# Performance work log

Hardware: AMD Instinct MI355X
Metric: run time of the kernel (lower is better)

The kernel has to match this reference:

```python
import jax, jax.numpy as jnp
import numpy as np

B, S, N, M = 64, 512, 512, 128   # batch, sensory_size, state_size, motor_size
UNFOLDS = 6
DT = 0.1  # elapsed_time


def _gate(v, mu, sigma):
    # piecewise-linear 'sigmoid': clip((v - mu + sigma) / (2 sigma), 0, 1)
    # v: [B, P] -> [B, P, 1] broadcast against [P, N]
    return jnp.clip((v[..., None] - mu + sigma) / (2.0 * sigma), 0.0, 1.0)


def setup_inputs() -> dict:
    key = jax.random.key(0)
    ks = jax.random.split(key, 12)
    u = lambda k, sh, lo, hi: jax.random.uniform(k, sh, jnp.float32, lo, hi)
    inputs = jax.random.normal(ks[0], (B, S), dtype=jnp.float32)
    states = jax.random.normal(ks[1], (B, N), dtype=jnp.float32) * 0.1
    # parameters per _init_ranges
    tau = u(ks[2], (N,), 0.001, 2.0)
    b = u(ks[3], (N,), -0.2, 0.2)
    erev = jnp.where(jax.random.bernoulli(ks[4], 0.8, (N, N)), 1.0, -1.0).astype(jnp.float32)
    w = u(ks[5], (N, N), 0.001, 1.0)
    sigma = jnp.full((N, N), 0.5, jnp.float32)
    mu = jnp.full((N, N), 0.5, jnp.float32)
    sensory_erev = jnp.where(jax.random.bernoulli(ks[6], 0.8, (S, N)), 1.0, -1.0).astype(jnp.float32)
    sensory_w = u(ks[7], (S, N), 0.001, 1.0)
    sensory_sigma = jnp.full((S, N), 0.5, jnp.float32)
    sensory_mu = jnp.full((S, N), 0.5, jnp.float32)
    sparsity_mask = jax.random.bernoulli(ks[8], 0.3, (N, N)).astype(jnp.float32)
    sensory_sparsity_mask = jax.random.bernoulli(ks[9], 0.3, (S, N)).astype(jnp.float32)
    input_w = jnp.ones((S,), jnp.float32)
    input_b = jnp.zeros((S,), jnp.float32)
    output_w = jnp.ones((M,), jnp.float32)
    output_b = jnp.zeros((M,), jnp.float32)
    return dict(inputs=inputs, states=states, tau=tau, b=b, erev=erev, w=w,
                sigma=sigma, mu=mu, sensory_erev=sensory_erev, sensory_w=sensory_w,
                sensory_sigma=sensory_sigma, sensory_mu=sensory_mu,
                sparsity_mask=sparsity_mask, sensory_sparsity_mask=sensory_sparsity_mask,
                input_w=input_w, input_b=input_b, output_w=output_w, output_b=output_b)


def reference(inputs, states, tau, b, erev, w, sigma, mu,
              sensory_erev, sensory_w, sensory_sigma, sensory_mu,
              sparsity_mask, sensory_sparsity_mask,
              input_w, input_b, output_w, output_b):
    # input mapping (affine)
    x = inputs * input_w + input_b                                   # [B, S]
    # sensory synapses, computed once
    sa = _gate(x, sensory_mu, sensory_sigma) * sensory_sparsity_mask  # [B, S, N]
    s_rev = jnp.einsum('bsn,sn->bn', sa, sensory_erev)               # [B, N]
    s_w = jnp.einsum('bsn,sn->bn', sa, sensory_w)                    # [B, N]
    delta = DT / UNFOLDS

    def step(v, _):
        g = _gate(v, mu, sigma) * sparsity_mask                      # [B, N, N]
        sum_rev = jnp.einsum('bij,ij->bj', g, erev) + s_rev + b      # sum over presynaptic i
        sum_w = jnp.einsum('bij,ij->bj', g, w) + s_w
        k = 1.0 / (1.0 + sum_w)
        taun = tau * k
        q = taun / (taun + delta)
        v_new = q * v + (1.0 - q) * k * sum_rev
        return v_new, None

    v, _ = jax.lax.scan(step, states, None, length=UNFOLDS)
    # output mapping: slice last M neurons (M < N), then affine
    out = v[:, -M:] * output_w + output_b                            # [B, M]
    return out, v
```

## Files before the change

kernel.cpp:

```cpp
#include <hip/hip_runtime.h>

constexpr int cB = 64, cS = 512, cN = 512, cM = 128, cUNF = 6;
constexpr float cDELTA = 0.016666666666666666f;

constexpr int KB = 4;
constexpr int JT = 32;
constexpr int NJT = cN / JT;
constexpr int NT = 1024;
constexpr int NW = NT / 64;
constexpr int NB = (cB / KB) * NJT;

constexpr int ILEN = 8;
constexpr int SLEN = 16;

constexpr int SM_EW    = 0;
constexpr int SM_STAGE = cN * JT * 2;
constexpr int SM_REDR  = SM_STAGE + cN * KB;
constexpr int SM_REDW  = SM_REDR + KB * NW * JT;
constexpr int SM_FLOATS = SM_REDW + KB * NW * JT;
constexpr size_t SMEM_BYTES = (size_t)SM_FLOATS * 4;

constexpr size_t OFF_EWT = 0;
constexpr size_t OFF_SRB = (size_t)cN * cN * 2;
constexpr size_t OFF_SW  = OFF_SRB + (size_t)cB * cN;
constexpr size_t OFF_VA  = OFF_SW  + (size_t)cB * cN;
constexpr size_t OFF_VB  = OFF_VA  + (size_t)cB * cN;
constexpr size_t OFF_CTR = OFF_VB  + (size_t)cB * cN;
constexpr int CTR_INTS = 256 + 16;

__device__ __forceinline__ float clamp01(float x) {
    return __builtin_amdgcn_fmed3f(x, 0.0f, 1.0f);
}

__global__ __launch_bounds__(NT)
void k_prep(const float* __restrict__ inputs, const float* __restrict__ bias,
            const float* __restrict__ erev,  const float* __restrict__ wgt,
            const float* __restrict__ sigma, const float* __restrict__ mu,
            const float* __restrict__ serev, const float* __restrict__ swgt,
            const float* __restrict__ ssigma,const float* __restrict__ smu,
            const float* __restrict__ mask,  const float* __restrict__ smask,
            const float* __restrict__ inw,   const float* __restrict__ inb,
            float* __restrict__ ws)
{
    float2* EWt  = (float2*)(ws + OFF_EWT);
    float*  srb  = ws + OFF_SRB;
    float*  swS  = ws + OFF_SW;
    int*    ctr  = (int*)(ws + OFF_CTR);
    int*    flags = ctr + 256;

    const int tid = threadIdx.x, bid = blockIdx.x;
    const int bg = bid >> 4, jt = bid & (NJT - 1);
    const int b0 = bg * KB, j0 = jt * JT;
    const int jl = tid & (JT - 1), ic = tid >> 5;
    const int wv_id = tid >> 6, lane = tid & 63;
    const int j = j0 + jl;

    __shared__ float xsh[cS * KB];
    __shared__ float redR[KB * NW * JT];
    __shared__ float redW[KB * NW * JT];

    {
        int idx = bid * NT + tid;
        int i = idx >> 9, jj = idx & (cN - 1);
        int jtt = jj >> 5, jjl = jj & (JT - 1);
        float mk = mask[idx];
        EWt[(size_t)jtt * (cN * JT) + i * JT + jjl] =
            make_float2(erev[idx] * mk, wgt[idx] * mk);
        if (mk != 0.0f && !((sigma[idx] == 0.5f) && (mu[idx] == 0.5f)))
            atomicOr(&flags[jtt], 1);
    }

#pragma unroll
    for (int r = 0; r < (cS * KB) / NT; ++r) {
        int t = tid + r * NT;
        int bb = t & 3, s = t >> 2;
        xsh[t] = fmaf(inputs[(b0 + bb) * cS + s], inw[s], inb[s]);
    }
    __syncthreads();

    {
        float aR[KB] = {0.f, 0.f, 0.f, 0.f}, aW[KB] = {0.f, 0.f, 0.f, 0.f};
        int idx = (ic * SLEN) * cN + j;
        int xo  = (ic * SLEN) * KB;
#pragma unroll 4
        for (int ii = 0; ii < SLEN; ++ii, idx += cN, xo += KB) {
            float sg = ssigma[idx];
            float a  = 0.5f / sg;
            float c  = fmaf(-smu[idx], a, 0.5f);
            float mk = smask[idx];
            float e  = serev[idx] * mk;
            float wv = swgt[idx] * mk;
            const float4 xv = *(const float4*)&xsh[xo];
            float g;
            g = clamp01(fmaf(xv.x, a, c)); aR[0] = fmaf(g, e, aR[0]); aW[0] = fmaf(g, wv, aW[0]);
            g = clamp01(fmaf(xv.y, a, c)); aR[1] = fmaf(g, e, aR[1]); aW[1] = fmaf(g, wv, aW[1]);
            g = clamp01(fmaf(xv.z, a, c)); aR[2] = fmaf(g, e, aR[2]); aW[2] = fmaf(g, wv, aW[2]);
            g = clamp01(fmaf(xv.w, a, c)); aR[3] = fmaf(g, e, aR[3]); aW[3] = fmaf(g, wv, aW[3]);
        }
#pragma unroll
        for (int b = 0; b < KB; ++b) {
            aR[b] += __shfl_xor(aR[b], 32, 64);
            aW[b] += __shfl_xor(aW[b], 32, 64);
        }
        if (lane < JT) {
#pragma unroll
            for (int b = 0; b < KB; ++b) {
                redR[(b * NW + wv_id) * JT + jl] = aR[b];
                redW[(b * NW + wv_id) * JT + jl] = aW[b];
            }
        }
    }
    __syncthreads();

    if (tid < JT * KB) {
        int jj = tid & (JT - 1), bb = tid >> 5;
        float r = 0.f, wv = 0.f;
#pragma unroll
        for (int w = 0; w < NW; ++w) {
            r  += redR[(bb * NW + w) * JT + jj];
            wv += redW[(bb * NW + w) * JT + jj];
        }
        int jg = j0 + jj;
        int gidx = (b0 + bb) * cN + jg;
        srb[gidx] = r + bias[jg];
        swS[gidx] = wv;
    }
}

__global__ __launch_bounds__(NT)
void k_main(const float* __restrict__ states, const float* __restrict__ tau,
            const float* __restrict__ sigma,  const float* __restrict__ mu,
            const float* __restrict__ outw,   const float* __restrict__ outb,
            float* __restrict__ out, float* __restrict__ ws)
{
    extern __shared__ float smem[];
    float*  ewlf  = smem + SM_EW;
    float*  stage = smem + SM_STAGE;
    float*  redR  = smem + SM_REDR;
    float*  redW  = smem + SM_REDW;

    const float* srb = ws + OFF_SRB;
    const float* swS = ws + OFF_SW;
    float* vA  = ws + OFF_VA;
    float* vB  = ws + OFF_VB;
    int*   ctr = (int*)(ws + OFF_CTR);

    const int tid = threadIdx.x, bid = blockIdx.x;
    const int jt = (bid & 7) * 2 + ((bid >> 3) & 1);
    const int bg = bid >> 4;
    const int b0 = bg * KB, j0 = jt * JT;
    const int jp = tid & 15;
    const int ic = tid >> 4;
    const int wv_id = tid >> 6, lane = tid & 63;
    int* barU  = ctr + bg * 16;
    const int* flags = ctr + 256;

    {
        const float4* gsrc = (const float4*)(ws + OFF_EWT) + (size_t)jt * (cN * JT / 2);
        float4* ldst = (float4*)ewlf;
#pragma unroll 2
        for (int k = 0; k < 8; ++k)
            ldst[k * NT + tid] = gsrc[k * NT + tid];
    }
    const int fast = (flags[jt] == 0);

    float my_srb = 0.f, my_sw = 0.f, my_tau = 0.f, my_ow = 0.f, my_ob = 0.f;
    int my_gidx = 0, my_mi = -1;
    if (tid < JT * KB) {
        int jj = tid & (JT - 1), bb = tid >> 5;
        int jg = j0 + jj;
        my_gidx = (b0 + bb) * cN + jg;
        my_srb  = srb[my_gidx];
        my_sw   = swS[my_gidx];
        my_tau  = tau[jg];
        if (jg >= cN - cM) {
            int m = jg - (cN - cM);
            my_ow = outw[m]; my_ob = outb[m];
            my_mi = (b0 + bb) * cM + m;
        }
    }

    const float* vin = states;
    for (int u = 0; u < cUNF; ++u) {
        float* vout = (u == cUNF - 1) ? (out + cB * cM) : ((u & 1) ? vA : vB);

#pragma unroll
        for (int r = 0; r < (cN * KB) / NT; ++r) {
            int t = tid + r * NT;
            int bb = t & 3, ii = t >> 2;
            float vvv = __hip_atomic_load(&vin[(b0 + bb) * cN + ii],
                                          __ATOMIC_RELAXED, __HIP_MEMORY_SCOPE_AGENT);
            stage[t] = fast ? clamp01(vvv) : vvv;
        }
        __syncthreads();

        float vold = 0.f;
        if (tid < JT * KB)
            vold = __hip_atomic_load(&vin[my_gidx],
                                     __ATOMIC_RELAXED, __HIP_MEMORY_SCOPE_AGENT);

        float aR0[KB] = {0,0,0,0}, aW0[KB] = {0,0,0,0};
        float aR1[KB] = {0,0,0,0}, aW1[KB] = {0,0,0,0};
        const float4* ew4 = (const float4*)ewlf;
        if (fast) {
#pragma unroll
            for (int ii = 0; ii < ILEN; ++ii) {
                int i = ic * ILEN + ii;
                const float4 ew = ew4[i * 16 + jp];
                const float4 g4 = *(const float4*)&stage[i * KB];
                aR0[0] = fmaf(g4.x, ew.x, aR0[0]); aW0[0] = fmaf(g4.x, ew.y, aW0[0]);
                aR0[1] = fmaf(g4.y, ew.x, aR0[1]); aW0[1] = fmaf(g4.y, ew.y, aW0[1]);
                aR0[2] = fmaf(g4.z, ew.x, aR0[2]); aW0[2] = fmaf(g4.z, ew.y, aW0[2]);
                aR0[3] = fmaf(g4.w, ew.x, aR0[3]); aW0[3] = fmaf(g4.w, ew.y, aW0[3]);
                aR1[0] = fmaf(g4.x, ew.z, aR1[0]); aW1[0] = fmaf(g4.x, ew.w, aW1[0]);
                aR1[1] = fmaf(g4.y, ew.z, aR1[1]); aW1[1] = fmaf(g4.y, ew.w, aW1[1]);
                aR1[2] = fmaf(g4.z, ew.z, aR1[2]); aW1[2] = fmaf(g4.z, ew.w, aW1[2]);
                aR1[3] = fmaf(g4.w, ew.z, aR1[3]); aW1[3] = fmaf(g4.w, ew.w, aW1[3]);
            }
        } else {
            int j2 = j0 + jp * 2;
#pragma unroll 2
            for (int ii = 0; ii < ILEN; ++ii) {
                int i = ic * ILEN + ii;
                const float4 ew = ew4[i * 16 + jp];
                float sg0 = sigma[i * cN + j2],     mu0 = mu[i * cN + j2];
                float sg1 = sigma[i * cN + j2 + 1], mu1 = mu[i * cN + j2 + 1];
                float a0 = 0.5f / sg0, c0 = fmaf(-mu0, a0, 0.5f);
                float a1 = 0.5f / sg1, c1 = fmaf(-mu1, a1, 0.5f);
                const float4 v4 = *(const float4*)&stage[i * KB];
                float g;
                g = clamp01(fmaf(v4.x, a0, c0)); aR0[0] = fmaf(g, ew.x, aR0[0]); aW0[0] = fmaf(g, ew.y, aW0[0]);
                g = clamp01(fmaf(v4.y, a0, c0)); aR0[1] = fmaf(g, ew.x, aR0[1]); aW0[1] = fmaf(g, ew.y, aW0[1]);
                g = clamp01(fmaf(v4.z, a0, c0)); aR0[2] = fmaf(g, ew.x, aR0[2]); aW0[2] = fmaf(g, ew.y, aW0[2]);
                g = clamp01(fmaf(v4.w, a0, c0)); aR0[3] = fmaf(g, ew.x, aR0[3]); aW0[3] = fmaf(g, ew.y, aW0[3]);
                g = clamp01(fmaf(v4.x, a1, c1)); aR1[0] = fmaf(g, ew.z, aR1[0]); aW1[0] = fmaf(g, ew.w, aW1[0]);
                g = clamp01(fmaf(v4.y, a1, c1)); aR1[1] = fmaf(g, ew.z, aR1[1]); aW1[1] = fmaf(g, ew.w, aW1[1]);
                g = clamp01(fmaf(v4.z, a1, c1)); aR1[2] = fmaf(g, ew.z, aR1[2]); aW1[2] = fmaf(g, ew.w, aW1[2]);
                g = clamp01(fmaf(v4.w, a1, c1)); aR1[3] = fmaf(g, ew.z, aR1[3]); aW1[3] = fmaf(g, ew.w, aW1[3]);
            }
        }
#pragma unroll
        for (int b = 0; b < KB; ++b) {
            aR0[b] += __shfl_xor(aR0[b], 16, 64); aR0[b] += __shfl_xor(aR0[b], 32, 64);
            aW0[b] += __shfl_xor(aW0[b], 16, 64); aW0[b] += __shfl_xor(aW0[b], 32, 64);
            aR1[b] += __shfl_xor(aR1[b], 16, 64); aR1[b] += __shfl_xor(aR1[b], 32, 64);
            aW1[b] += __shfl_xor(aW1[b], 16, 64); aW1[b] += __shfl_xor(aW1[b], 32, 64);
        }
        if (lane < 16) {
#pragma unroll
            for (int b = 0; b < KB; ++b) {
                *(float2*)&redR[(b * NW + wv_id) * JT + lane * 2] = make_float2(aR0[b], aR1[b]);
                *(float2*)&redW[(b * NW + wv_id) * JT + lane * 2] = make_float2(aW0[b], aW1[b]);
            }
        }
        __syncthreads();

        if (tid < JT * KB) {
            int jj = tid & (JT - 1), bb = tid >> 5;
            float r = 0.f, wv = 0.f;
#pragma unroll
            for (int w = 0; w < NW; ++w) {
                r  += redR[(bb * NW + w) * JT + jj];
                wv += redW[(bb * NW + w) * JT + jj];
            }
            r  += my_srb;
            wv += my_sw;
            float k    = 1.0f / (1.0f + wv);
            float taun = my_tau * k;
            float inv  = 1.0f / (taun + cDELTA);
            float vn   = (taun * inv) * vold + (cDELTA * inv) * k * r;
            if (u == cUNF - 1) {
                vout[my_gidx] = vn;
                if (my_mi >= 0) out[my_mi] = fmaf(vn, my_ow, my_ob);
            } else {
                __hip_atomic_store(&vout[my_gidx], vn,
                                   __ATOMIC_RELAXED, __HIP_MEMORY_SCOPE_AGENT);
            }
        }

        if (u < cUNF - 1) {
            __syncthreads();
            if (tid == 0) {
                __hip_atomic_fetch_add(barU, 1, __ATOMIC_RELAXED, __HIP_MEMORY_SCOPE_AGENT);
                const int target = NJT * (u + 1);
                while (__hip_atomic_load(barU, __ATOMIC_RELAXED, __HIP_MEMORY_SCOPE_AGENT) < target)
                    __builtin_amdgcn_s_sleep(1);
            }
            __syncthreads();
            vin = (u & 1) ? vA : vB;
        }
    }
}

extern "C" void kernel_launch(void* const* d_in, const int* in_sizes, int n_in,
                              void* d_out, int out_size, void* d_ws, size_t ws_size,
                              hipStream_t stream)
{
    const float* inputs = (const float*)d_in[0];
    const float* states = (const float*)d_in[1];
    const float* tau    = (const float*)d_in[2];
    const float* bias   = (const float*)d_in[3];
    const float* erev   = (const float*)d_in[4];
    const float* wgt    = (const float*)d_in[5];
    const float* sigma  = (const float*)d_in[6];
    const float* mu     = (const float*)d_in[7];
    const float* serev  = (const float*)d_in[8];
    const float* swgt   = (const float*)d_in[9];
    const float* ssigma = (const float*)d_in[10];
    const float* smu    = (const float*)d_in[11];
    const float* mask   = (const float*)d_in[12];
    const float* smask  = (const float*)d_in[13];
    const float* inw    = (const float*)d_in[14];
    const float* inb    = (const float*)d_in[15];
    const float* outw   = (const float*)d_in[16];
    const float* outb   = (const float*)d_in[17];
    float* out = (float*)d_out;
    float* ws  = (float*)d_ws;

    hipFuncSetAttribute((const void*)k_main,
                        hipFuncAttributeMaxDynamicSharedMemorySize,
                        (int)SMEM_BYTES);

    hipMemsetAsync(ws + OFF_CTR, 0, CTR_INTS * sizeof(int), stream);

    k_prep<<<NB, NT, 0, stream>>>(inputs, bias, erev, wgt, sigma, mu,
                                  serev, swgt, ssigma, smu, mask, smask,
                                  inw, inb, ws);

    k_main<<<NB, NT, SMEM_BYTES, stream>>>(states, tau, sigma, mu,
                                           outw, outb, out, ws);
}
```

Measured before the change: 144.3 us.

## Read synapse weights from global/L2 instead of staging them in LDS

k_main no longer copies its 128KB erev/w tile into dynamic shared memory. It reads the float2 weights straight from global memory (expected to stay resident in L2) and keeps only small static LDS buffers. The inner loop changes to one j column per thread over 16 presynaptic rows, and k_prep writes the weights with relaxed atomic stores. This removes the per-block LDS fill and the large LDS footprint, which should allow more blocks per CU, but every unfold step now re-reads weights from cache hierarchy instead of LDS.

```diff
diff --git a/kernel.cpp b/kernel.cpp
--- a/kernel.cpp
+++ b/kernel.cpp
@@ -1,4 +1,5 @@
 #include <hip/hip_runtime.h>
+#include <string.h>
 
 constexpr int cB = 64, cS = 512, cN = 512, cM = 128, cUNF = 6;
 constexpr float cDELTA = 0.016666666666666666f;
@@ -9,16 +10,8 @@
 constexpr int NT = 1024;
 constexpr int NW = NT / 64;
 constexpr int NB = (cB / KB) * NJT;
-
-constexpr int ILEN = 8;
+constexpr int ILEN = 16;
 constexpr int SLEN = 16;
-
-constexpr int SM_EW    = 0;
-constexpr int SM_STAGE = cN * JT * 2;
-constexpr int SM_REDR  = SM_STAGE + cN * KB;
-constexpr int SM_REDW  = SM_REDR + KB * NW * JT;
-constexpr int SM_FLOATS = SM_REDW + KB * NW * JT;
-constexpr size_t SMEM_BYTES = (size_t)SM_FLOATS * 4;
 
 constexpr size_t OFF_EWT = 0;
 constexpr size_t OFF_SRB = (size_t)cN * cN * 2;
@@ -64,8 +57,12 @@
         int i = idx >> 9, jj = idx & (cN - 1);
         int jtt = jj >> 5, jjl = jj & (JT - 1);
         float mk = mask[idx];
-        EWt[(size_t)jtt * (cN * JT) + i * JT + jjl] =
-            make_float2(erev[idx] * mk, wgt[idx] * mk);
+        float2 ew = make_float2(erev[idx] * mk, wgt[idx] * mk);
+        unsigned long long bits;
+        memcpy(&bits, &ew, 8);
+        __hip_atomic_store(
+            (unsigned long long*)&EWt[(size_t)jtt * (cN * JT) + i * JT + jjl],
+            bits, __ATOMIC_RELAXED, __HIP_MEMORY_SCOPE_AGENT);
         if (mk != 0.0f && !((sigma[idx] == 0.5f) && (mu[idx] == 0.5f)))
             atomicOr(&flags[jtt], 1);
     }
@@ -105,8 +102,8 @@
         if (lane < JT) {
 #pragma unroll
             for (int b = 0; b < KB; ++b) {
-                redR[(b * NW + wv_id) * JT + jl] = aR[b];
-                redW[(b * NW + wv_id) * JT + jl] = aW[b];
+                redR[(b * NW + wv_id) * JT + lane] = aR[b];
+                redW[(b * NW + wv_id) * JT + lane] = aW[b];
             }
         }
     }
@@ -127,18 +124,12 @@
     }
 }
 
-__global__ __launch_bounds__(NT)
+__global__ __launch_bounds__(NT, 4)
 void k_main(const float* __restrict__ states, const float* __restrict__ tau,
             const float* __restrict__ sigma,  const float* __restrict__ mu,
             const float* __restrict__ outw,   const float* __restrict__ outb,
             float* __restrict__ out, float* __restrict__ ws)
 {
-    extern __shared__ float smem[];
-    float*  ewlf  = smem + SM_EW;
-    float*  stage = smem + SM_STAGE;
-    float*  redR  = smem + SM_REDR;
-    float*  redW  = smem + SM_REDW;
-
     const float* srb = ws + OFF_SRB;
     const float* swS = ws + OFF_SW;
     float* vA  = ws + OFF_VA;
@@ -149,19 +140,17 @@
     const int jt = (bid & 7) * 2 + ((bid >> 3) & 1);
     const int bg = bid >> 4;
     const int b0 = bg * KB, j0 = jt * JT;
-    const int jp = tid & 15;
-    const int ic = tid >> 4;
+    const int jl = tid & (JT - 1), ic = tid >> 5;
     const int wv_id = tid >> 6, lane = tid & 63;
-    int* barU  = ctr + bg * 16;
+    int* barU = ctr + bg * 16;
     const int* flags = ctr + 256;
 
-    {
-        const float4* gsrc = (const float4*)(ws + OFF_EWT) + (size_t)jt * (cN * JT / 2);
-        float4* ldst = (float4*)ewlf;
-#pragma unroll 2
-        for (int k = 0; k < 8; ++k)
-            ldst[k * NT + tid] = gsrc[k * NT + tid];
-    }
+    const float2* ews = (const float2*)(ws + OFF_EWT) + (size_t)jt * (cN * JT);
+
+    __shared__ float stage[cN * KB];
+    __shared__ float redR[KB * NW * JT];
+    __shared__ float redW[KB * NW * JT];
+
     const int fast = (flags[jt] == 0);
 
     float my_srb = 0.f, my_sw = 0.f, my_tau = 0.f, my_ow = 0.f, my_ob = 0.f;
@@ -199,58 +188,48 @@
             vold = __hip_atomic_load(&vin[my_gidx],
                                      __ATOMIC_RELAXED, __HIP_MEMORY_SCOPE_AGENT);
 
-        float aR0[KB] = {0,0,0,0}, aW0[KB] = {0,0,0,0};
-        float aR1[KB] = {0,0,0,0}, aW1[KB] = {0,0,0,0};
-        const float4* ew4 = (const float4*)ewlf;
+        float aR[KB] = {0.f, 0.f, 0.f, 0.f}, aW[KB] = {0.f, 0.f, 0.f, 0.f};
         if (fast) {
-#pragma unroll
-            for (int ii = 0; ii < ILEN; ++ii) {
-                int i = ic * ILEN + ii;
-                const float4 ew = ew4[i * 16 + jp];
-                const float4 g4 = *(const float4*)&stage[i * KB];
-                aR0[0] = fmaf(g4.x, ew.x, aR0[0]); aW0[0] = fmaf(g4.x, ew.y, aW0[0]);
-                aR0[1] = fmaf(g4.y, ew.x, aR0[1]); aW0[1] = fmaf(g4.y, ew.y, aW0[1]);
-                aR0[2] = fmaf(g4.z, ew.x, aR0[2]); aW0[2] = fmaf(g4.z, ew.y, aW0[2]);
-                aR0[3] = fmaf(g4.w, ew.x, aR0[3]); aW0[3] = fmaf(g4.w, ew.y, aW0[3]);
-                aR1[0] = fmaf(g4.x, ew.z, aR1[0]); aW1[0] = fmaf(g4.x, ew.w, aW1[0]);
-                aR1[1] = fmaf(g4.y, ew.z, aR1[1]); aW1[1] = fmaf(g4.y, ew.w, aW1[1]);
-                aR1[2] = fmaf(g4.z, ew.z, aR1[2]); aW1[2] = fmaf(g4.z, ew.w, aW1[2]);
-                aR1[3] = fmaf(g4.w, ew.z, aR1[3]); aW1[3] = fmaf(g4.w, ew.w, aW1[3]);
+            int eo = (ic * ILEN) * JT + jl;
+            int vo = (ic * ILEN) * KB;
+#pragma unroll 8
+            for (int ii = 0; ii < ILEN; ++ii, eo += JT, vo += KB) {
+                const float2 ew = ews[eo];
+                const float4 g4 = *(const float4*)&stage[vo];
+                aR[0] = fmaf(g4.x, ew.x, aR[0]); aW[0] = fmaf(g4.x, ew.y, aW[0]);
+                aR[1] = fmaf(g4.y, ew.x, aR[1]); aW[1] = fmaf(g4.y, ew.y, aW[1]);
+                aR[2] = fmaf(g4.z, ew.x, aR[2]); aW[2] = fmaf(g4.z, ew.y, aW[2]);
+                aR[3] = fmaf(g4.w, ew.x, aR[3]); aW[3] = fmaf(g4.w, ew.y, aW[3]);
             }
         } else {
-            int j2 = j0 + jp * 2;
-#pragma unroll 2
-            for (int ii = 0; ii < ILEN; ++ii) {
-                int i = ic * ILEN + ii;
-                const float4 ew = ew4[i * 16 + jp];
-                float sg0 = sigma[i * cN + j2],     mu0 = mu[i * cN + j2];
-                float sg1 = sigma[i * cN + j2 + 1], mu1 = mu[i * cN + j2 + 1];
-                float a0 = 0.5f / sg0, c0 = fmaf(-mu0, a0, 0.5f);
-                float a1 = 0.5f / sg1, c1 = fmaf(-mu1, a1, 0.5f);
-                const float4 v4 = *(const float4*)&stage[i * KB];
+            int j    = j0 + jl;
+            int idx  = (ic * ILEN) * cN + j;
+            int eo   = (ic * ILEN) * JT + jl;
+            int vo   = (ic * ILEN) * KB;
+#pragma unroll 4
+            for (int ii = 0; ii < ILEN; ++ii, idx += cN, eo += JT, vo += KB) {
+                float sg = sigma[idx];
+                float a  = 0.5f / sg;
+                float c  = fmaf(-mu[idx], a, 0.5f);
+                const float2 ew = ews[eo];
+                const float4 v4 = *(const float4*)&stage[vo];
                 float g;
-                g = clamp01(fmaf(v4.x, a0, c0)); aR0[0] = fmaf(g, ew.x, aR0[0]); aW0[0] = fmaf(g, ew.y, aW0[0]);
-                g = clamp01(fmaf(v4.y, a0, c0)); aR0[1] = fmaf(g, ew.x, aR0[1]); aW0[1] = fmaf(g, ew.y, aW0[1]);
-                g = clamp01(fmaf(v4.z, a0, c0)); aR0[2] = fmaf(g, ew.x, aR0[2]); aW0[2] = fmaf(g, ew.y, aW0[2]);
-                g = clamp01(fmaf(v4.w, a0, c0)); aR0[3] = fmaf(g, ew.x, aR0[3]); aW0[3] = fmaf(g, ew.y, aW0[3]);
-                g = clamp01(fmaf(v4.x, a1, c1)); aR1[0] = fmaf(g, ew.z, aR1[0]); aW1[0] = fmaf(g, ew.w, aW1[0]);
-                g = clamp01(fmaf(v4.y, a1, c1)); aR1[1] = fmaf(g, ew.z, aR1[1]); aW1[1] = fmaf(g, ew.w, aW1[1]);
-                g = clamp01(fmaf(v4.z, a1, c1)); aR1[2] = fmaf(g, ew.z, aR1[2]); aW1[2] = fmaf(g, ew.w, aW1[2]);
-                g = clamp01(fmaf(v4.w, a1, c1)); aR1[3] = fmaf(g, ew.z, aR1[3]); aW1[3] = fmaf(g, ew.w, aW1[3]);
+                g = clamp01(fmaf(v4.x, a, c)); aR[0] = fmaf(g, ew.x, aR[0]); aW[0] = fmaf(g, ew.y, aW[0]);
+                g = clamp01(fmaf(v4.y, a, c)); aR[1] = fmaf(g, ew.x, aR[1]); aW[1] = fmaf(g, ew.y, aW[1]);
+                g = clamp01(fmaf(v4.z, a, c)); aR[2] = fmaf(g, ew.x, aR[2]); aW[2] = fmaf(g, ew.y, aW[2]);
+                g = clamp01(fmaf(v4.w, a, c)); aR[3] = fmaf(g, ew.x, aR[3]); aW[3] = fmaf(g, ew.y, aW[3]);
             }
         }
 #pragma unroll
         for (int b = 0; b < KB; ++b) {
-            aR0[b] += __shfl_xor(aR0[b], 16, 64); aR0[b] += __shfl_xor(aR0[b], 32, 64);
-            aW0[b] += __shfl_xor(aW0[b], 16, 64); aW0[b] += __shfl_xor(aW0[b], 32, 64);
-            aR1[b] += __shfl_xor(aR1[b], 16, 64); aR1[b] += __shfl_xor(aR1[b], 32, 64);
-            aW1[b] += __shfl_xor(aW1[b], 16, 64); aW1[b] += __shfl_xor(aW1[b], 32, 64);
-        }
-        if (lane < 16) {
+            aR[b] += __shfl_xor(aR[b], 32, 64);
+            aW[b] += __shfl_xor(aW[b], 32, 64);
+        }
+        if (lane < JT) {
 #pragma unroll
             for (int b = 0; b < KB; ++b) {
-                *(float2*)&redR[(b * NW + wv_id) * JT + lane * 2] = make_float2(aR0[b], aR1[b]);
-                *(float2*)&redW[(b * NW + wv_id) * JT + lane * 2] = make_float2(aW0[b], aW1[b]);
+                redR[(b * NW + wv_id) * JT + lane] = aR[b];
+                redW[(b * NW + wv_id) * JT + lane] = aW[b];
             }
         }
         __syncthreads();
@@ -317,16 +296,12 @@
     float* out = (float*)d_out;
     float* ws  = (float*)d_ws;
 
-    hipFuncSetAttribute((const void*)k_main,
-                        hipFuncAttributeMaxDynamicSharedMemorySize,
-                        (int)SMEM_BYTES);
-
     hipMemsetAsync(ws + OFF_CTR, 0, CTR_INTS * sizeof(int), stream);
 
     k_prep<<<NB, NT, 0, stream>>>(inputs, bias, erev, wgt, sigma, mu,
                                   serev, swgt, ssigma, smu, mask, smask,
                                   inw, inb, ws);
 
-    k_main<<<NB, NT, SMEM_BYTES, stream>>>(states, tau, sigma, mu,
-                                           outw, outb, out, ws);
+    k_main<<<NB, NT, 0, stream>>>(states, tau, sigma, mu,
+                                  outw, outb, out, ws);
 }
```

After: 127.5 us. -11.7%, faster.
